# Kernel tuning notes

Measured on AMD Instinct MI355X. Metric: run time of the kernel, lower is better.

Reference implementation:

```python
import jax, jax.numpy as jnp
import numpy as np

B, D, P, C = 4096, 512, 256, 8
LAMBDA = 1.0


def setup_inputs() -> dict:
    key = jax.random.key(0)
    k1, k2, k3, k4 = jax.random.split(key, 4)
    x = jax.random.normal(k1, (B, D), dtype=jnp.float32)
    y = jax.random.randint(k2, (B,), 0, C, dtype=jnp.int32)
    prototypes = jax.random.normal(k3, (P, D), dtype=jnp.float32)
    # omega initialized as eye + 0.01*randn per class, like the torch module
    omega = jnp.eye(D, dtype=jnp.float32)[None] + 0.01 * jax.random.normal(k4, (C, D, D), dtype=jnp.float32)
    prototype_labels = (jnp.arange(P, dtype=jnp.int32) % C).astype(jnp.int32)
    return {"x": x, "y": y, "prototypes": prototypes, "omega": omega, "prototype_labels": prototype_labels}


def reference(x, y, prototypes, omega, prototype_labels):
    # transformed inputs per class: tx[c,b,:] = omega[c] @ x[b]
    tx = jnp.einsum('cij,bj->cbi', omega, x)                     # [C,B,D]
    # transformed prototypes under every class omega, then pick each
    # prototype's own class matrix: tp[p,:] = omega[label[p]] @ w[p]
    tp_all = jnp.einsum('cij,pj->cpi', omega, prototypes)        # [C,P,D]
    tp = tp_all[prototype_labels, jnp.arange(P)]                 # [P,D]
    # squared distances via expansion ||a-b||^2 = |a|^2 + |b|^2 - 2ab
    dots = jnp.einsum('cbd,pd->cbp', tx, tp)                     # [C,B,P]
    x2 = jnp.sum(tx * tx, axis=-1)                               # [C,B]
    p2 = jnp.sum(tp * tp, axis=-1)                               # [P]
    dist_all = x2[:, :, None] + p2[None, None, :] - 2.0 * dots   # [C,B,P]
    # each prototype uses the omega of its own class
    dist = dist_all[prototype_labels, :, jnp.arange(P)].T        # [B,P]
    same = prototype_labels[None, :] == y[:, None]               # [B,P]
    inf = jnp.float32(jnp.inf)
    pos = jnp.min(jnp.where(same, dist, inf), axis=1)            # [B]
    neg = jnp.min(jnp.where(same, inf, dist), axis=1)            # [B]
    mu = (pos - neg) / (pos + neg)
    loss = jnp.mean(jax.nn.sigmoid(LAMBDA * mu))
    loss = loss + 0.01 * jnp.linalg.norm(omega.reshape(-1))
    return loss
```

## Files before the change

kernel.cpp:

```cpp
#include <hip/hip_runtime.h>
#include <math.h>

typedef unsigned short ushort_t;
typedef __attribute__((ext_vector_type(8))) short short8;
typedef __attribute__((ext_vector_type(4))) float f32x4;

#define B_N 4096
#define D_N 512
#define P_N 256
#define C_N 8

#define ACC_OFF   0
#define P2G_OFF   256
#define X2_OFF    1280
#define XB_OFF    132352
#define OMB_OFF   (XB_OFF + B_N*D_N*2)
#define TPG_OFF   (OMB_OFF + C_N*D_N*D_N*2)
#define UG_OFF    (TPG_OFF + P_N*D_N*2)
#define OMBT_OFF  (UG_OFF + P_N*D_N*2)
#define DOTS_OFF  OMBT_OFF

#define MFMA16(a, b, c) __builtin_amdgcn_mfma_f32_16x16x32_bf16(a, b, c, 0, 0, 0)

__device__ inline ushort_t f2bf(float f) {
    union { float f; unsigned u; } v; v.f = f;
    unsigned r = v.u + 0x7FFFu + ((v.u >> 16) & 1u);
    return (ushort_t)(r >> 16);
}

__device__ __forceinline__ void gll16(const ushort_t* g, ushort_t* l) {
    __builtin_amdgcn_global_load_lds((const __attribute__((address_space(1))) void*)g,
                                     (__attribute__((address_space(3))) void*)l, 16, 0, 0);
}

__global__ void k_cast_x(const float* __restrict__ x, ushort_t* __restrict__ xb) {
    int idx = blockIdx.x * 256 + threadIdx.x;
    const float4* x4 = (const float4*)x;
    float4 a = x4[idx * 2], b = x4[idx * 2 + 1];
    union { ushort_t s[8]; uint4 v; } o;
    o.s[0] = f2bf(a.x); o.s[1] = f2bf(a.y); o.s[2] = f2bf(a.z); o.s[3] = f2bf(a.w);
    o.s[4] = f2bf(b.x); o.s[5] = f2bf(b.y); o.s[6] = f2bf(b.z); o.s[7] = f2bf(b.w);
    ((uint4*)xb)[idx] = o.v;
}

__global__ void k_cast_om(const float* __restrict__ omega, ushort_t* __restrict__ omb,
                          ushort_t* __restrict__ ombT, float* __restrict__ oss) {
    int c = blockIdx.z, r0 = blockIdx.y * 64, c0 = blockIdx.x * 64;
    __shared__ ushort_t T[64][72];
    __shared__ float red[4];
    int t = threadIdx.x;
    int r = t >> 2, seg = t & 3;
    const float* src = omega + ((size_t)c * D_N + r0 + r) * D_N + c0 + seg * 16;
    float4 v0 = ((const float4*)src)[0], v1 = ((const float4*)src)[1];
    float4 v2 = ((const float4*)src)[2], v3 = ((const float4*)src)[3];
    float s = v0.x*v0.x + v0.y*v0.y + v0.z*v0.z + v0.w*v0.w
            + v1.x*v1.x + v1.y*v1.y + v1.z*v1.z + v1.w*v1.w
            + v2.x*v2.x + v2.y*v2.y + v2.z*v2.z + v2.w*v2.w
            + v3.x*v3.x + v3.y*v3.y + v3.z*v3.z + v3.w*v3.w;
    union { ushort_t s[16]; uint4 v[2]; } o;
    float vv[16] = {v0.x,v0.y,v0.z,v0.w, v1.x,v1.y,v1.z,v1.w,
                    v2.x,v2.y,v2.z,v2.w, v3.x,v3.y,v3.z,v3.w};
    #pragma unroll
    for (int j = 0; j < 16; ++j) o.s[j] = f2bf(vv[j]);
    uint4* dst = (uint4*)(omb + ((size_t)c * D_N + r0 + r) * D_N + c0 + seg * 16);
    dst[0] = o.v[0]; dst[1] = o.v[1];
    #pragma unroll
    for (int j = 0; j < 16; ++j) T[seg * 16 + j][r] = o.s[j];
    __syncthreads();
    int jr = t >> 2, sg2 = t & 3;
    uint4 w0 = *(uint4*)&T[jr][sg2 * 16];
    uint4 w1 = *(uint4*)&T[jr][sg2 * 16 + 8];
    uint4* dstT = (uint4*)(ombT + ((size_t)c * D_N + c0 + jr) * D_N + r0 + sg2 * 16);
    dstT[0] = w0; dstT[1] = w1;
    #pragma unroll
    for (int off = 32; off > 0; off >>= 1) s += __shfl_down(s, off);
    if ((t & 63) == 0) red[t >> 6] = s;
    __syncthreads();
    if (t == 0) atomicAdd(oss, red[0] + red[1] + red[2] + red[3]);
}

__global__ __launch_bounds__(256) void k_tp(const float* __restrict__ prot,
                                            const ushort_t* __restrict__ omb,
                                            ushort_t* __restrict__ tpg,
                                            float* __restrict__ p2g) {
    int i0 = blockIdx.x * 64, c = blockIdx.y;
    __shared__ ushort_t As[32][72];
    __shared__ ushort_t Bs[64][72];
    int t = threadIdx.x, w = t >> 6, lane = t & 63;
    int g = lane >> 4, cl = lane & 15;
    f32x4 acc[2] = {{0,0,0,0},{0,0,0,0}};
    for (int k0 = 0; k0 < D_N; k0 += 64) {
        __syncthreads();
        {
            int m = t >> 3, seg = t & 7;
            const float* ap = prot + ((size_t)(c + 8 * m)) * D_N + k0 + seg * 8;
            float4 u0 = ((const float4*)ap)[0], u1 = ((const float4*)ap)[1];
            union { ushort_t s[8]; uint4 v; } o;
            o.s[0]=f2bf(u0.x); o.s[1]=f2bf(u0.y); o.s[2]=f2bf(u0.z); o.s[3]=f2bf(u0.w);
            o.s[4]=f2bf(u1.x); o.s[5]=f2bf(u1.y); o.s[6]=f2bf(u1.z); o.s[7]=f2bf(u1.w);
            *(uint4*)&As[m][seg * 8] = o.v;
        }
        {
            int r = t >> 2, sg = t & 3;
            const uint4* bp = (const uint4*)(omb + ((size_t)c * D_N + i0 + r) * D_N + k0 + sg * 16);
            *(uint4*)&Bs[r][sg * 16] = bp[0];
            *(uint4*)&Bs[r][sg * 16 + 8] = bp[1];
        }
        __syncthreads();
        #pragma unroll
        for (int kk = 0; kk < 2; ++kk) {
            int koff = kk * 32 + g * 8;
            short8 bfr = *(const short8*)&Bs[w * 16 + cl][koff];
            #pragma unroll
            for (int mt = 0; mt < 2; ++mt) {
                short8 afr = *(const short8*)&As[mt * 16 + cl][koff];
                acc[mt] = MFMA16(afr, bfr, acc[mt]);
            }
        }
    }
    #pragma unroll
    for (int mt = 0; mt < 2; ++mt)
        #pragma unroll
        for (int reg = 0; reg < 4; ++reg) {
            float v = acc[mt][reg];
            int m = mt * 16 + g * 4 + reg;
            int i = i0 + w * 16 + cl;
            tpg[((size_t)c * 32 + m) * D_N + i] = f2bf(v);
            float s = v * v;
            s += __shfl_xor(s, 1); s += __shfl_xor(s, 2);
            s += __shfl_xor(s, 4); s += __shfl_xor(s, 8);
            if (cl == 0) atomicAdd(&p2g[c * 32 + m], s);
        }
}

__global__ __launch_bounds__(256) void k_u(const ushort_t* __restrict__ tpg,
                                           const ushort_t* __restrict__ ombT,
                                           ushort_t* __restrict__ ug) {
    int j0 = blockIdx.x * 64, c = blockIdx.y;
    __shared__ ushort_t As[32][72];
    __shared__ ushort_t Bs[64][72];
    int t = threadIdx.x, w = t >> 6, lane = t & 63;
    int g = lane >> 4, cl = lane & 15;
    f32x4 acc[2] = {{0,0,0,0},{0,0,0,0}};
    for (int k0 = 0; k0 < D_N; k0 += 64) {
        __syncthreads();
        {
            int m = t >> 3, seg = t & 7;
            *(uint4*)&As[m][seg * 8] =
                *(const uint4*)(tpg + ((size_t)c * 32 + m) * D_N + k0 + seg * 8);
        }
        {
            int r = t >> 2, sg = t & 3;
            const uint4* bp = (const uint4*)(ombT + ((size_t)c * D_N + j0 + r) * D_N + k0 + sg * 16);
            *(uint4*)&Bs[r][sg * 16] = bp[0];
            *(uint4*)&Bs[r][sg * 16 + 8] = bp[1];
        }
        __syncthreads();
        #pragma unroll
        for (int kk = 0; kk < 2; ++kk) {
            int koff = kk * 32 + g * 8;
            short8 bfr = *(const short8*)&Bs[w * 16 + cl][koff];
            #pragma unroll
            for (int mt = 0; mt < 2; ++mt) {
                short8 afr = *(const short8*)&As[mt * 16 + cl][koff];
                acc[mt] = MFMA16(afr, bfr, acc[mt]);
            }
        }
    }
    #pragma unroll
    for (int mt = 0; mt < 2; ++mt)
        #pragma unroll
        for (int reg = 0; reg < 4; ++reg) {
            int m = mt * 16 + g * 4 + reg;
            int j = j0 + w * 16 + cl;
            ug[((size_t)c * 32 + m) * D_N + j] = f2bf(acc[mt][reg]);
        }
}

__global__ __launch_bounds__(256, 4) void k_x2(const ushort_t* __restrict__ xb,
                                               const ushort_t* __restrict__ omb,
                                               float* __restrict__ x2) {
    int i0 = blockIdx.x * 128;
    int c  = blockIdx.y;
    int b0 = blockIdx.z * 128;
    __shared__ ushort_t Xs[128][64];
    __shared__ ushort_t Os[128][64];
    __shared__ float red[128][2];
    int t = threadIdx.x, w = t >> 6, lane = t & 63;
    int qr = w >> 1, qc = w & 1;
    int g = lane >> 4, cl = lane & 15;
    int lrow = lane >> 3, lpos = lane & 7;
    f32x4 acc[4][4];
    #pragma unroll
    for (int mt = 0; mt < 4; ++mt)
        #pragma unroll
        for (int nt = 0; nt < 4; ++nt) acc[mt][nt] = (f32x4){0,0,0,0};

    for (int k0 = 0; k0 < D_N; k0 += 64) {
        __syncthreads();
        #pragma unroll
        for (int i = 0; i < 4; ++i) {
            int rb = w * 32 + i * 8;
            int r  = rb + lrow;
            int cg = (lpos + r) & 7;
            gll16(xb + (size_t)(b0 + r) * D_N + k0 + cg * 8, &Xs[rb][0]);
            gll16(omb + ((size_t)c * D_N + i0 + r) * D_N + k0 + cg * 8, &Os[rb][0]);
        }
        __syncthreads();
        #pragma unroll
        for (int kk = 0; kk < 2; ++kk) {
            int p8 = ((kk * 4 + g - cl) & 7) * 8;
            short8 a[4], b[4];
            #pragma unroll
            for (int mt = 0; mt < 4; ++mt)
                a[mt] = *(const short8*)&Xs[qr * 64 + mt * 16 + cl][p8];
            #pragma unroll
            for (int nt = 0; nt < 4; ++nt)
                b[nt] = *(const short8*)&Os[qc * 64 + nt * 16 + cl][p8];
            #pragma unroll
            for (int mt = 0; mt < 4; ++mt)
                #pragma unroll
                for (int nt = 0; nt < 4; ++nt)
                    acc[mt][nt] = MFMA16(a[mt], b[nt], acc[mt][nt]);
        }
    }
    #pragma unroll
    for (int mt = 0; mt < 4; ++mt)
        #pragma unroll
        for (int reg = 0; reg < 4; ++reg) {
            float s = 0.f;
            #pragma unroll
            for (int nt = 0; nt < 4; ++nt) s += acc[mt][nt][reg] * acc[mt][nt][reg];
            s += __shfl_xor(s, 1); s += __shfl_xor(s, 2);
            s += __shfl_xor(s, 4); s += __shfl_xor(s, 8);
            if (cl == 0) red[qr * 64 + mt * 16 + g * 4 + reg][qc] = s;
        }
    __syncthreads();
    if (t < 128) atomicAdd(&x2[(size_t)(b0 + t) * C_N + c], red[t][0] + red[t][1]);
}

__global__ __launch_bounds__(256) void k_dots(const ushort_t* __restrict__ xb,
                                              const ushort_t* __restrict__ ug,
                                              float* __restrict__ dots) {
    int b0 = blockIdx.x * 64, q0 = blockIdx.y * 64;
    __shared__ ushort_t Xs[64][72];
    __shared__ ushort_t Us[64][72];
    int t = threadIdx.x, w = t >> 6, lane = t & 63;
    int qr = w >> 1, qc = w & 1;
    int g = lane >> 4, cl = lane & 15;
    f32x4 acc[2][2];
    #pragma unroll
    for (int mt = 0; mt < 2; ++mt)
        #pragma unroll
        for (int nt = 0; nt < 2; ++nt) acc[mt][nt] = (f32x4){0,0,0,0};
    for (int k0 = 0; k0 < D_N; k0 += 64) {
        __syncthreads();
        {
            int r = t >> 2, sg = t & 3;
            const uint4* xp = (const uint4*)(xb + (size_t)(b0 + r) * D_N + k0 + sg * 16);
            *(uint4*)&Xs[r][sg * 16] = xp[0];
            *(uint4*)&Xs[r][sg * 16 + 8] = xp[1];
            const uint4* up = (const uint4*)(ug + (size_t)(q0 + r) * D_N + k0 + sg * 16);
            *(uint4*)&Us[r][sg * 16] = up[0];
            *(uint4*)&Us[r][sg * 16 + 8] = up[1];
        }
        __syncthreads();
        #pragma unroll
        for (int kk = 0; kk < 2; ++kk) {
            int koff = kk * 32 + g * 8;
            short8 a[2], b[2];
            #pragma unroll
            for (int mt = 0; mt < 2; ++mt)
                a[mt] = *(const short8*)&Xs[qr * 32 + mt * 16 + cl][koff];
            #pragma unroll
            for (int nt = 0; nt < 2; ++nt)
                b[nt] = *(const short8*)&Us[qc * 32 + nt * 16 + cl][koff];
            #pragma unroll
            for (int mt = 0; mt < 2; ++mt)
                #pragma unroll
                for (int nt = 0; nt < 2; ++nt)
                    acc[mt][nt] = MFMA16(a[mt], b[nt], acc[mt][nt]);
        }
    }
    #pragma unroll
    for (int mt = 0; mt < 2; ++mt)
        #pragma unroll
        for (int nt = 0; nt < 2; ++nt)
            #pragma unroll
            for (int reg = 0; reg < 4; ++reg) {
                int b = b0 + qr * 32 + mt * 16 + g * 4 + reg;
                int q = q0 + qc * 32 + nt * 16 + cl;
                dots[(size_t)b * P_N + q] = acc[mt][nt][reg];
            }
}

__global__ void k_mu(const float* __restrict__ dots, const float* __restrict__ x2,
                     const float* __restrict__ p2g, const int* __restrict__ y,
                     float* __restrict__ acc) {
    int t = threadIdx.x, w = t >> 6, lane = t & 63;
    int b = blockIdx.x * 4 + w;
    __shared__ float red[4];
    int yb = y[b];
    float pos = INFINITY, neg = INFINITY;
    #pragma unroll
    for (int j = 0; j < 4; ++j) {
        int q = lane + j * 64;
        int lab = q >> 5;
        float dist = x2[(size_t)b * C_N + lab] + p2g[q] - 2.f * dots[(size_t)b * P_N + q];
        if (lab == yb) pos = fminf(pos, dist);
        else           neg = fminf(neg, dist);
    }
    #pragma unroll
    for (int off = 32; off > 0; off >>= 1) {
        pos = fminf(pos, __shfl_xor(pos, off));
        neg = fminf(neg, __shfl_xor(neg, off));
    }
    if (lane == 0) {
        float mu = (pos - neg) / (pos + neg);
        red[w] = 1.f / (1.f + expf(-mu));
    }
    __syncthreads();
    if (t == 0) atomicAdd(acc, red[0] + red[1] + red[2] + red[3]);
}

__global__ void k_final(const float* __restrict__ accs, float* __restrict__ out) {
    out[0] = accs[0] * (1.f / (float)B_N) + 0.01f * sqrtf(accs[1]);
}

extern "C" void kernel_launch(void* const* d_in, const int* in_sizes, int n_in,
                              void* d_out, int out_size, void* d_ws, size_t ws_size,
                              hipStream_t stream) {
    (void)in_sizes; (void)n_in; (void)out_size; (void)ws_size;
    const float* x     = (const float*)d_in[0];
    const int*   y     = (const int*)d_in[1];
    const float* prot  = (const float*)d_in[2];
    const float* omega = (const float*)d_in[3];

    char* ws = (char*)d_ws;
    float*    accs = (float*)(ws + ACC_OFF);
    float*    p2g  = (float*)(ws + P2G_OFF);
    float*    x2   = (float*)(ws + X2_OFF);
    ushort_t* xb   = (ushort_t*)(ws + XB_OFF);
    ushort_t* omb  = (ushort_t*)(ws + OMB_OFF);
    ushort_t* tpg  = (ushort_t*)(ws + TPG_OFF);
    ushort_t* ug   = (ushort_t*)(ws + UG_OFF);
    ushort_t* ombT = (ushort_t*)(ws + OMBT_OFF);
    float*    dots = (float*)(ws + DOTS_OFF);

    (void)hipMemsetAsync(ws, 0, XB_OFF, stream);
    k_cast_x <<<B_N * D_N / 8 / 256, 256, 0, stream>>>(x, xb);
    k_cast_om<<<dim3(8, 8, C_N), 256, 0, stream>>>(omega, omb, ombT, accs + 1);
    k_tp     <<<dim3(8, C_N), 256, 0, stream>>>(prot, omb, tpg, p2g);
    k_u      <<<dim3(8, C_N), 256, 0, stream>>>(tpg, ombT, ug);
    k_x2     <<<dim3(4, C_N, B_N / 128), 256, 0, stream>>>(xb, omb, x2);
    k_dots   <<<dim3(B_N / 64, P_N / 64), 256, 0, stream>>>(xb, ug, dots);
    k_mu     <<<B_N / 4, 256, 0, stream>>>(dots, x2, p2g, y, accs);
    k_final  <<<1, 1, 0, stream>>>(accs, (float*)d_out);
}
```

Baseline: 141.4 us.

## Fuse x2 and dots GEMMs into one kernel with per-class min epilogue

Merges the x2 GEMM and the dots GEMM into one launch, using an extra blockIdx.x slice for the dots work. The dots path reduces p2-2*dot to a per-class minimum in its epilogue, so the full B×P dots matrix is never written or read back. Both paths switch to double-buffered 32-wide K tiles loaded with async global-to-LDS copies and a swizzled layout. k_mu then only reads 8 values per row, at the cost of heterogeneous blocks in one grid and smaller K steps with more barriers.

```diff
diff --git a/kernel.cpp b/kernel.cpp
--- a/kernel.cpp
+++ b/kernel.cpp
@@ -18,7 +18,7 @@
 #define TPG_OFF   (OMB_OFF + C_N*D_N*D_N*2)
 #define UG_OFF    (TPG_OFF + P_N*D_N*2)
 #define OMBT_OFF  (UG_OFF + P_N*D_N*2)
-#define DOTS_OFF  OMBT_OFF
+#define MINB_OFF  OMBT_OFF
 
 #define MFMA16(a, b, c) __builtin_amdgcn_mfma_f32_16x16x32_bf16(a, b, c, 0, 0, 0)
 
@@ -177,148 +177,177 @@
         }
 }
 
-__global__ __launch_bounds__(256, 4) void k_x2(const ushort_t* __restrict__ xb,
-                                               const ushort_t* __restrict__ omb,
-                                               float* __restrict__ x2) {
-    int i0 = blockIdx.x * 128;
+__global__ __launch_bounds__(256, 4) void k_x2d(const ushort_t* __restrict__ xb,
+                                                const ushort_t* __restrict__ omb,
+                                                const ushort_t* __restrict__ ug,
+                                                const float* __restrict__ p2g,
+                                                float* __restrict__ x2,
+                                                float* __restrict__ minb) {
     int c  = blockIdx.y;
     int b0 = blockIdx.z * 128;
-    __shared__ ushort_t Xs[128][64];
-    __shared__ ushort_t Os[128][64];
+    int t = threadIdx.x, w = t >> 6, lane = t & 63;
+    int g = lane >> 4, cl = lane & 15;
+    int srow = lane >> 2, spos = lane & 3;
+
+    __shared__ ushort_t Xs[2][128][32];
+    __shared__ ushort_t Os[2][128][32];
     __shared__ float red[128][2];
-    int t = threadIdx.x, w = t >> 6, lane = t & 63;
-    int qr = w >> 1, qc = w & 1;
-    int g = lane >> 4, cl = lane & 15;
-    int lrow = lane >> 3, lpos = lane & 7;
-    f32x4 acc[4][4];
-    #pragma unroll
-    for (int mt = 0; mt < 4; ++mt)
-        #pragma unroll
-        for (int nt = 0; nt < 4; ++nt) acc[mt][nt] = (f32x4){0,0,0,0};
-
-    for (int k0 = 0; k0 < D_N; k0 += 64) {
-        __syncthreads();
-        #pragma unroll
-        for (int i = 0; i < 4; ++i) {
-            int rb = w * 32 + i * 8;
-            int r  = rb + lrow;
-            int cg = (lpos + r) & 7;
-            gll16(xb + (size_t)(b0 + r) * D_N + k0 + cg * 8, &Xs[rb][0]);
-            gll16(omb + ((size_t)c * D_N + i0 + r) * D_N + k0 + cg * 8, &Os[rb][0]);
-        }
-        __syncthreads();
-        #pragma unroll
-        for (int kk = 0; kk < 2; ++kk) {
-            int p8 = ((kk * 4 + g - cl) & 7) * 8;
+
+    if (blockIdx.x < 4) {
+        int i0 = blockIdx.x * 128;
+        int qr = w >> 1, qc = w & 1;
+        f32x4 acc[4][4];
+        #pragma unroll
+        for (int mt = 0; mt < 4; ++mt)
+            #pragma unroll
+            for (int nt = 0; nt < 4; ++nt) acc[mt][nt] = (f32x4){0,0,0,0};
+        #pragma unroll
+        for (int i = 0; i < 2; ++i) {
+            int rb = w * 32 + i * 16;
+            int r  = rb + srow;
+            int cg = (spos + r) & 3;
+            gll16(xb + (size_t)(b0 + r) * D_N + cg * 8, &Xs[0][rb][0]);
+            gll16(omb + ((size_t)c * D_N + i0 + r) * D_N + cg * 8, &Os[0][rb][0]);
+        }
+        __syncthreads();
+        for (int s = 0; s < 16; ++s) {
+            int cb = s & 1, nb = cb ^ 1;
+            if (s < 15) {
+                int k1 = (s + 1) * 32;
+                #pragma unroll
+                for (int i = 0; i < 2; ++i) {
+                    int rb = w * 32 + i * 16;
+                    int r  = rb + srow;
+                    int cg = (spos + r) & 3;
+                    gll16(xb + (size_t)(b0 + r) * D_N + k1 + cg * 8, &Xs[nb][rb][0]);
+                    gll16(omb + ((size_t)c * D_N + i0 + r) * D_N + k1 + cg * 8, &Os[nb][rb][0]);
+                }
+            }
             short8 a[4], b[4];
             #pragma unroll
-            for (int mt = 0; mt < 4; ++mt)
-                a[mt] = *(const short8*)&Xs[qr * 64 + mt * 16 + cl][p8];
-            #pragma unroll
-            for (int nt = 0; nt < 4; ++nt)
-                b[nt] = *(const short8*)&Os[qc * 64 + nt * 16 + cl][p8];
+            for (int mt = 0; mt < 4; ++mt) {
+                int r = qr * 64 + mt * 16 + cl;
+                a[mt] = *(const short8*)&Xs[cb][r][((g - r) & 3) * 8];
+            }
+            #pragma unroll
+            for (int nt = 0; nt < 4; ++nt) {
+                int r = qc * 64 + nt * 16 + cl;
+                b[nt] = *(const short8*)&Os[cb][r][((g - r) & 3) * 8];
+            }
             #pragma unroll
             for (int mt = 0; mt < 4; ++mt)
                 #pragma unroll
                 for (int nt = 0; nt < 4; ++nt)
                     acc[mt][nt] = MFMA16(a[mt], b[nt], acc[mt][nt]);
-        }
-    }
-    #pragma unroll
-    for (int mt = 0; mt < 4; ++mt)
-        #pragma unroll
-        for (int reg = 0; reg < 4; ++reg) {
-            float s = 0.f;
-            #pragma unroll
-            for (int nt = 0; nt < 4; ++nt) s += acc[mt][nt][reg] * acc[mt][nt][reg];
-            s += __shfl_xor(s, 1); s += __shfl_xor(s, 2);
-            s += __shfl_xor(s, 4); s += __shfl_xor(s, 8);
-            if (cl == 0) red[qr * 64 + mt * 16 + g * 4 + reg][qc] = s;
-        }
-    __syncthreads();
-    if (t < 128) atomicAdd(&x2[(size_t)(b0 + t) * C_N + c], red[t][0] + red[t][1]);
-}
-
-__global__ __launch_bounds__(256) void k_dots(const ushort_t* __restrict__ xb,
-                                              const ushort_t* __restrict__ ug,
-                                              float* __restrict__ dots) {
-    int b0 = blockIdx.x * 64, q0 = blockIdx.y * 64;
-    __shared__ ushort_t Xs[64][72];
-    __shared__ ushort_t Us[64][72];
-    int t = threadIdx.x, w = t >> 6, lane = t & 63;
-    int qr = w >> 1, qc = w & 1;
-    int g = lane >> 4, cl = lane & 15;
-    f32x4 acc[2][2];
-    #pragma unroll
-    for (int mt = 0; mt < 2; ++mt)
-        #pragma unroll
-        for (int nt = 0; nt < 2; ++nt) acc[mt][nt] = (f32x4){0,0,0,0};
-    for (int k0 = 0; k0 < D_N; k0 += 64) {
-        __syncthreads();
-        {
-            int r = t >> 2, sg = t & 3;
-            const uint4* xp = (const uint4*)(xb + (size_t)(b0 + r) * D_N + k0 + sg * 16);
-            *(uint4*)&Xs[r][sg * 16] = xp[0];
-            *(uint4*)&Xs[r][sg * 16 + 8] = xp[1];
-            const uint4* up = (const uint4*)(ug + (size_t)(q0 + r) * D_N + k0 + sg * 16);
-            *(uint4*)&Us[r][sg * 16] = up[0];
-            *(uint4*)&Us[r][sg * 16 + 8] = up[1];
-        }
-        __syncthreads();
-        #pragma unroll
-        for (int kk = 0; kk < 2; ++kk) {
-            int koff = kk * 32 + g * 8;
+            __syncthreads();
+        }
+        #pragma unroll
+        for (int mt = 0; mt < 4; ++mt)
+            #pragma unroll
+            for (int reg = 0; reg < 4; ++reg) {
+                float s = 0.f;
+                #pragma unroll
+                for (int nt = 0; nt < 4; ++nt) s += acc[mt][nt][reg] * acc[mt][nt][reg];
+                s += __shfl_xor(s, 1); s += __shfl_xor(s, 2);
+                s += __shfl_xor(s, 4); s += __shfl_xor(s, 8);
+                if (cl == 0) red[qr * 64 + mt * 16 + g * 4 + reg][qc] = s;
+            }
+        __syncthreads();
+        if (t < 128) atomicAdd(&x2[(size_t)(b0 + t) * C_N + c], red[t][0] + red[t][1]);
+    } else {
+        f32x4 acc[2][2];
+        #pragma unroll
+        for (int mt = 0; mt < 2; ++mt)
+            #pragma unroll
+            for (int nt = 0; nt < 2; ++nt) acc[mt][nt] = (f32x4){0,0,0,0};
+        #pragma unroll
+        for (int i = 0; i < 2; ++i) {
+            int rb = w * 32 + i * 16;
+            int r  = rb + srow;
+            int cg = (spos + r) & 3;
+            gll16(xb + (size_t)(b0 + r) * D_N + cg * 8, &Xs[0][rb][0]);
+        }
+        if (w < 2) {
+            int rb = w * 16;
+            int r  = rb + srow;
+            int cg = (spos + r) & 3;
+            gll16(ug + ((size_t)c * 32 + r) * D_N + cg * 8, &Os[0][rb][0]);
+        }
+        __syncthreads();
+        for (int s = 0; s < 16; ++s) {
+            int cb = s & 1, nb = cb ^ 1;
+            if (s < 15) {
+                int k1 = (s + 1) * 32;
+                #pragma unroll
+                for (int i = 0; i < 2; ++i) {
+                    int rb = w * 32 + i * 16;
+                    int r  = rb + srow;
+                    int cg = (spos + r) & 3;
+                    gll16(xb + (size_t)(b0 + r) * D_N + k1 + cg * 8, &Xs[nb][rb][0]);
+                }
+                if (w < 2) {
+                    int rb = w * 16;
+                    int r  = rb + srow;
+                    int cg = (spos + r) & 3;
+                    gll16(ug + ((size_t)c * 32 + r) * D_N + k1 + cg * 8, &Os[nb][rb][0]);
+                }
+            }
             short8 a[2], b[2];
             #pragma unroll
-            for (int mt = 0; mt < 2; ++mt)
-                a[mt] = *(const short8*)&Xs[qr * 32 + mt * 16 + cl][koff];
-            #pragma unroll
-            for (int nt = 0; nt < 2; ++nt)
-                b[nt] = *(const short8*)&Us[qc * 32 + nt * 16 + cl][koff];
+            for (int mt = 0; mt < 2; ++mt) {
+                int r = w * 32 + mt * 16 + cl;
+                a[mt] = *(const short8*)&Xs[cb][r][((g - r) & 3) * 8];
+            }
+            #pragma unroll
+            for (int nt = 0; nt < 2; ++nt) {
+                int r = nt * 16 + cl;
+                b[nt] = *(const short8*)&Os[cb][r][((g - r) & 3) * 8];
+            }
             #pragma unroll
             for (int mt = 0; mt < 2; ++mt)
                 #pragma unroll
                 for (int nt = 0; nt < 2; ++nt)
                     acc[mt][nt] = MFMA16(a[mt], b[nt], acc[mt][nt]);
-        }
+            __syncthreads();
+        }
+        #pragma unroll
+        for (int mt = 0; mt < 2; ++mt)
+            #pragma unroll
+            for (int reg = 0; reg < 4; ++reg) {
+                float v = INFINITY;
+                #pragma unroll
+                for (int nt = 0; nt < 2; ++nt) {
+                    int q = c * 32 + nt * 16 + cl;
+                    v = fminf(v, p2g[q] - 2.f * acc[mt][nt][reg]);
+                }
+                v = fminf(v, __shfl_xor(v, 1)); v = fminf(v, __shfl_xor(v, 2));
+                v = fminf(v, __shfl_xor(v, 4)); v = fminf(v, __shfl_xor(v, 8));
+                if (cl == 0)
+                    minb[(size_t)(b0 + w * 32 + mt * 16 + g * 4 + reg) * C_N + c] = v;
+            }
     }
-    #pragma unroll
-    for (int mt = 0; mt < 2; ++mt)
-        #pragma unroll
-        for (int nt = 0; nt < 2; ++nt)
-            #pragma unroll
-            for (int reg = 0; reg < 4; ++reg) {
-                int b = b0 + qr * 32 + mt * 16 + g * 4 + reg;
-                int q = q0 + qc * 32 + nt * 16 + cl;
-                dots[(size_t)b * P_N + q] = acc[mt][nt][reg];
-            }
-}
-
-__global__ void k_mu(const float* __restrict__ dots, const float* __restrict__ x2,
-                     const float* __restrict__ p2g, const int* __restrict__ y,
-                     float* __restrict__ acc) {
-    int t = threadIdx.x, w = t >> 6, lane = t & 63;
-    int b = blockIdx.x * 4 + w;
+}
+
+__global__ void k_mu(const float* __restrict__ x2, const float* __restrict__ minb,
+                     const int* __restrict__ y, float* __restrict__ acc) {
+    int t = threadIdx.x;
+    int b = blockIdx.x * 256 + t;
+    int yb = y[b];
+    float d[8];
+    #pragma unroll
+    for (int cc = 0; cc < 8; ++cc)
+        d[cc] = x2[(size_t)b * C_N + cc] + minb[(size_t)b * C_N + cc];
+    float pos = d[yb];
+    float neg = INFINITY;
+    #pragma unroll
+    for (int cc = 0; cc < 8; ++cc)
+        if (cc != yb) neg = fminf(neg, d[cc]);
+    float mu = (pos - neg) / (pos + neg);
+    float s = 1.f / (1.f + expf(-mu));
+    #pragma unroll
+    for (int off = 32; off > 0; off >>= 1) s += __shfl_down(s, off);
     __shared__ float red[4];
-    int yb = y[b];
-    float pos = INFINITY, neg = INFINITY;
-    #pragma unroll
-    for (int j = 0; j < 4; ++j) {
-        int q = lane + j * 64;
-        int lab = q >> 5;
-        float dist = x2[(size_t)b * C_N + lab] + p2g[q] - 2.f * dots[(size_t)b * P_N + q];
-        if (lab == yb) pos = fminf(pos, dist);
-        else           neg = fminf(neg, dist);
-    }
-    #pragma unroll
-    for (int off = 32; off > 0; off >>= 1) {
-        pos = fminf(pos, __shfl_xor(pos, off));
-        neg = fminf(neg, __shfl_xor(neg, off));
-    }
-    if (lane == 0) {
-        float mu = (pos - neg) / (pos + neg);
-        red[w] = 1.f / (1.f + expf(-mu));
-    }
+    if ((t & 63) == 0) red[t >> 6] = s;
     __syncthreads();
     if (t == 0) atomicAdd(acc, red[0] + red[1] + red[2] + red[3]);
 }
@@ -345,15 +374,14 @@
     ushort_t* tpg  = (ushort_t*)(ws + TPG_OFF);
     ushort_t* ug   = (ushort_t*)(ws + UG_OFF);
     ushort_t* ombT = (ushort_t*)(ws + OMBT_OFF);
-    float*    dots = (float*)(ws + DOTS_OFF);
+    float*    minb = (float*)(ws + MINB_OFF);
 
     (void)hipMemsetAsync(ws, 0, XB_OFF, stream);
     k_cast_x <<<B_N * D_N / 8 / 256, 256, 0, stream>>>(x, xb);
     k_cast_om<<<dim3(8, 8, C_N), 256, 0, stream>>>(omega, omb, ombT, accs + 1);
     k_tp     <<<dim3(8, C_N), 256, 0, stream>>>(prot, omb, tpg, p2g);
     k_u      <<<dim3(8, C_N), 256, 0, stream>>>(tpg, ombT, ug);
-    k_x2     <<<dim3(4, C_N, B_N / 128), 256, 0, stream>>>(xb, omb, x2);
-    k_dots   <<<dim3(B_N / 64, P_N / 64), 256, 0, stream>>>(xb, ug, dots);
-    k_mu     <<<B_N / 4, 256, 0, stream>>>(dots, x2, p2g, y, accs);
+    k_x2d    <<<dim3(5, C_N, B_N / 128), 256, 0, stream>>>(xb, omb, ug, p2g, x2, minb);
+    k_mu     <<<B_N / 256, 256, 0, stream>>>(x2, minb, y, accs);
     k_final  <<<1, 1, 0, stream>>>(accs, (float*)d_out);
 }
```

Result: faster. 135.4 us (-4.3%).
